# Performance work log

Measured on AMD Instinct MI355X. Metric: run time of the kernel, lower is better.

The kernel has to match this reference:

```python
import jax, jax.numpy as jnp
import numpy as np

B, N, F, FH, H = 8, 2048, 64, 64, 4
NEG_BIG = -1e10


def setup_inputs() -> dict:
    key = jax.random.key(0)
    k_x, k_a, k_w, k_as, k_an = jax.random.split(key, 5)
    X = jax.random.normal(k_x, (B, N, F), dtype=jnp.float32)
    A = (jax.random.uniform(k_a, (B, N, N)) < 0.1).astype(jnp.float32)
    A = jnp.maximum(A, jnp.eye(N, dtype=jnp.float32)[None])
    W = jax.random.normal(k_w, (H, F, FH), dtype=jnp.float32) * (1.0 / np.sqrt(F))
    b = jnp.zeros((H, FH), dtype=jnp.float32)
    a_self = jax.random.normal(k_as, (H, FH), dtype=jnp.float32) * (1.0 / np.sqrt(FH))
    a_neigh = jax.random.normal(k_an, (H, FH), dtype=jnp.float32) * (1.0 / np.sqrt(FH))
    return {"X": X, "A": A, "W": W, "b": b, "a_self": a_self, "a_neigh": a_neigh}


def reference(X, A, W, b, a_self, a_neigh):
    # per-head linear projection: [B,H,N,FH]
    feats = jnp.einsum("bnf,hfo->bhno", X, W)
    # additive attention logits: e_ij = leaky_relu(a_s.h_i + a_n.h_j)
    s_self = jnp.einsum("bhno,ho->bhn", feats, a_self)   # [B,H,N]
    s_neigh = jnp.einsum("bhno,ho->bhn", feats, a_neigh)  # [B,H,N]
    scores = s_self[:, :, :, None] + s_neigh[:, :, None, :]  # [B,H,N,N]
    scores = jax.nn.leaky_relu(scores, negative_slope=0.2)
    scores = scores + (1.0 - A)[:, None] * NEG_BIG  # adjacency mask
    attn = jax.nn.softmax(scores, axis=-1)
    # weighted aggregation + bias (dropouts are identity at inference)
    out = jnp.einsum("bhnm,bhmo->bhno", attn, feats) + b[None, :, None, :]
    # concat heads -> [B,N,H*FH], then activation
    Bd, Hd, Nd, Fd = out.shape
    out = jnp.transpose(out, (0, 2, 1, 3)).reshape(Bd, Nd, Hd * Fd)
    return jax.nn.relu(out)
```

## Files before the change

### kernel.cpp

```cpp
#include <hip/hip_runtime.h>
#include <hip/hip_bf16.h>
#include <stdint.h>

#define B_ 8
#define N_ 2048
#define F_ 64
#define FH_ 64
#define H_ 4
#define C_ (H_*FH_)
#define CHUNK 64
#define NCHUNK (N_/CHUNK)
#define LOG2E 1.44269504088896340736f

typedef short short8 __attribute__((ext_vector_type(8)));
typedef float f32x4 __attribute__((ext_vector_type(4)));

__device__ __forceinline__ short f2bf(float f) {
    __hip_bfloat16 h = __float2bfloat16(f);
    return __builtin_bit_cast(short, h);
}

__device__ __forceinline__ void async16(void* l, const void* g) {
    __builtin_amdgcn_global_load_lds((const __attribute__((address_space(1))) unsigned int*)g,
                                     (__attribute__((address_space(3))) unsigned int*)l, 16, 0, 0);
}
__device__ __forceinline__ void async4(void* l, const void* g) {
    __builtin_amdgcn_global_load_lds((const __attribute__((address_space(1))) unsigned int*)g,
                                     (__attribute__((address_space(3))) unsigned int*)l, 4, 0, 0);
}

__global__ __launch_bounds__(256) void k0_wt(const float* __restrict__ W,
                                             __hip_bfloat16* __restrict__ WT) {
    int idx = blockIdx.x * 256 + threadIdx.x;
    int h = idx >> 12, rem = idx & 4095, o = rem >> 6, f = rem & 63;
    WT[idx] = __float2bfloat16(W[(h * F_ + f) * FH_ + o]);
}

__global__ __launch_bounds__(256) void kp_pack(const float* __restrict__ A,
                                               unsigned long long* __restrict__ Amask) {
    const int wave = threadIdx.x >> 6, lane = threadIdx.x & 63;
    const int R = blockIdx.x * 4 + wave;
    const float* arow = A + (size_t)R * N_;
    unsigned long long* mrow = Amask + (size_t)R * (N_ / 64);
#pragma unroll
    for (int i = 0; i < 8; ++i) {
        float a0 = arow[i * 256 + lane];
        float a1 = arow[i * 256 + 64 + lane];
        float a2 = arow[i * 256 + 128 + lane];
        float a3 = arow[i * 256 + 192 + lane];
        unsigned long long m0 = __ballot(a0 != 0.0f);
        unsigned long long m1 = __ballot(a1 != 0.0f);
        unsigned long long m2 = __ballot(a2 != 0.0f);
        unsigned long long m3 = __ballot(a3 != 0.0f);
        if (lane == 0) {
            mrow[i * 4 + 0] = m0; mrow[i * 4 + 1] = m1;
            mrow[i * 4 + 2] = m2; mrow[i * 4 + 3] = m3;
        }
    }
}

__global__ __launch_bounds__(256) void k1_feats(const float* __restrict__ X,
                                                const __hip_bfloat16* __restrict__ WT,
                                                const float* __restrict__ a_self,
                                                const float* __restrict__ a_neigh,
                                                __hip_bfloat16* __restrict__ featsT,
                                                float* __restrict__ ss,
                                                float* __restrict__ sn) {
    __shared__ float a_lds[2][FH_];
    __shared__ __hip_bfloat16 c_lds[FH_ * 72];
    const int nb = blockIdx.x, h = blockIdx.y, b = blockIdx.z;
    const int tid = threadIdx.x;
    if (tid < 64)       a_lds[0][tid] = a_self[h * FH_ + tid];
    else if (tid < 128) a_lds[1][tid - 64] = a_neigh[h * FH_ + tid - 64];
    __syncthreads();

    const int wave = tid >> 6, lane = tid & 63;
    const int m = lane & 15, q = lane >> 4;
    const int nl = wave * 16 + m;
    const int n = nb * 64 + nl;
    f32x4 acc[4] = {};
#pragma unroll
    for (int ks = 0; ks < 2; ++ks) {
        const float* xp = X + ((size_t)(b * N_ + n)) * F_ + ks * 32 + q * 8;
        float4 x0 = *(const float4*)xp;
        float4 x1 = *(const float4*)(xp + 4);
        short8 bfrag;
        bfrag[0] = f2bf(x0.x); bfrag[1] = f2bf(x0.y);
        bfrag[2] = f2bf(x0.z); bfrag[3] = f2bf(x0.w);
        bfrag[4] = f2bf(x1.x); bfrag[5] = f2bf(x1.y);
        bfrag[6] = f2bf(x1.z); bfrag[7] = f2bf(x1.w);
#pragma unroll
        for (int ot = 0; ot < 4; ++ot) {
            short8 afrag = *(const short8*)(WT + ((size_t)(h * FH_ + ot * 16 + m)) * F_ + ks * 32 + q * 8);
            acc[ot] = __builtin_amdgcn_mfma_f32_16x16x32_bf16(afrag, bfrag, acc[ot], 0, 0, 0);
        }
    }
    float ssv = 0.f, snv = 0.f;
#pragma unroll
    for (int ot = 0; ot < 4; ++ot) {
#pragma unroll
        for (int r = 0; r < 4; ++r) {
            int orow = ot * 16 + q * 4 + r;
            float v = acc[ot][r];
            c_lds[orow * 72 + nl] = __float2bfloat16(v);
            ssv += v * a_lds[0][orow];
            snv += v * a_lds[1][orow];
        }
    }
    ssv += __shfl_xor(ssv, 16); ssv += __shfl_xor(ssv, 32);
    snv += __shfl_xor(snv, 16); snv += __shfl_xor(snv, 32);
    __syncthreads();
    {
        int o = tid >> 2, c = (tid & 3) * 16;
        const __hip_bfloat16* src = c_lds + o * 72 + c;
        __hip_bfloat16* dst = featsT + ((size_t)(b * H_ + h) * FH_ + o) * N_ + nb * 64 + c;
        *(uint4*)dst       = *(const uint4*)src;
        *(uint4*)(dst + 8) = *(const uint4*)(src + 8);
    }
    if (lane < 16) {
        size_t idx = ((size_t)(b * H_ + h)) * N_ + n;
        ss[idx] = ssv * LOG2E;
        sn[idx] = snv * LOG2E;
    }
}

__global__ __launch_bounds__(256, 4) void k3_attn(const unsigned int* __restrict__ Amask,
                                                  const __hip_bfloat16* __restrict__ featsT,
                                                  const float* __restrict__ ss,
                                                  const float* __restrict__ sn,
                                                  const float* __restrict__ bias,
                                                  float* __restrict__ out) {
    __shared__ __hip_bfloat16 fv_lds[2][64 * CHUNK];
    __shared__ unsigned int   mk_lds[2][64 * 2];
    __shared__ float e1_lds[N_];
    __shared__ float e2_lds[N_];

    const int tile = blockIdx.x, h = blockIdx.y, b = blockIdx.z;
    const int tid = threadIdx.x, wave = tid >> 6, lane = tid & 63;
    const int m = lane & 15, q = lane >> 4;
    const int rowtile = tile * 64;

    {
        const float4* snrow = (const float4*)(sn + ((size_t)(b * H_ + h)) * N_);
        float4* e1v = (float4*)e1_lds;
        float4* e2v = (float4*)e2_lds;
#pragma unroll
        for (int i = 0; i < 2; ++i) {
            int idx = tid + i * 256;
            float4 v = snrow[idx];
            float4 u1, u2;
            u1.x = exp2f(v.x); u1.y = exp2f(v.y); u1.z = exp2f(v.z); u1.w = exp2f(v.w);
            u2.x = exp2f(0.2f * v.x); u2.y = exp2f(0.2f * v.y);
            u2.z = exp2f(0.2f * v.z); u2.w = exp2f(0.2f * v.w);
            e1v[idx] = u1; e2v[idx] = u2;
        }
    }
    const float ssi = ss[((size_t)(b * H_ + h)) * N_ + rowtile + wave * 16 + m];
    const float e1i = exp2f(ssi), e2i = exp2f(0.2f * ssi);

    const __hip_bfloat16* fhead = featsT + ((size_t)(b * H_ + h)) * FH_ * N_;
    const unsigned int* mbase = Amask + ((size_t)(b * N_) + rowtile) * (N_ / 32);

    auto stage = [&](int c, int bufi) {
        const int cb = c * CHUNK;
#pragma unroll
        for (int i = 0; i < 2; ++i) {
            int base_unit = i * 256 + wave * 64;
            int unit = base_unit + lane;
            int o = unit >> 3, v = unit & 7;
            int u = v ^ (o & 7);
            async16(&fv_lds[bufi][base_unit * 8], fhead + (size_t)o * N_ + cb + u * 8);
        }
        if (wave < 2) {
            int base_unit = wave * 64;
            int unit = base_unit + lane;
            int row = unit >> 1, dw = unit & 1;
            async4(&mk_lds[bufi][base_unit], mbase + (size_t)row * (N_ / 32) + (cb >> 5) + dw);
        }
    };

    stage(0, 0);
    __syncthreads();

    f32x4 acc[2][4] = {};
    f32x4 accl[2] = {};
    short8 ones;
#pragma unroll
    for (int s = 0; s < 8; ++s) ones[s] = (short)0x3F80;

    for (int c = 0; c < NCHUNK; ++c) {
        const int cur = c & 1;
        if (c + 1 < NCHUNK) stage(c + 1, cur ^ 1);

        const int cg = c * CHUNK;
        float4 eA10 = *(const float4*)(e1_lds + cg + q * 8);
        float4 eA11 = *(const float4*)(e1_lds + cg + q * 8 + 4);
        float4 eB10 = *(const float4*)(e1_lds + cg + 32 + q * 8);
        float4 eB11 = *(const float4*)(e1_lds + cg + 32 + q * 8 + 4);
        float4 eA20 = *(const float4*)(e2_lds + cg + q * 8);
        float4 eA21 = *(const float4*)(e2_lds + cg + q * 8 + 4);
        float4 eB20 = *(const float4*)(e2_lds + cg + 32 + q * 8);
        float4 eB21 = *(const float4*)(e2_lds + cg + 32 + q * 8 + 4);
        short8 fA[4], fB[4];
#pragma unroll
        for (int ct = 0; ct < 4; ++ct) {
            int o = ct * 16 + m;
            fA[ct] = *(const short8*)(fv_lds[cur] + ((o << 3) + (q ^ (o & 7))) * 8);
            fB[ct] = *(const short8*)(fv_lds[cur] + ((o << 3) + ((4 + q) ^ (o & 7))) * 8);
        }
        unsigned int mA = mk_lds[cur][(wave * 16 + m) * 2];
        unsigned int mB = mk_lds[cur][(wave * 16 + m) * 2 + 1];

        float e1A[8] = {eA10.x, eA10.y, eA10.z, eA10.w, eA11.x, eA11.y, eA11.z, eA11.w};
        float e1B[8] = {eB10.x, eB10.y, eB10.z, eB10.w, eB11.x, eB11.y, eB11.z, eB11.w};
        float e2A[8] = {eA20.x, eA20.y, eA20.z, eA20.w, eA21.x, eA21.y, eA21.z, eA21.w};
        float e2B[8] = {eB20.x, eB20.y, eB20.z, eB20.w, eB21.x, eB21.y, eB21.z, eB21.w};

        short8 pA, pB;
#pragma unroll
        for (int s = 0; s < 8; ++s) {
            float vA = fmaxf(e1i * e1A[s], e2i * e2A[s]);
            float vB = fmaxf(e1i * e1B[s], e2i * e2B[s]);
            const int bit = q * 8 + s;
            pA[s] = (mA >> bit) & 1 ? f2bf(vA) : (short)0;
            pB[s] = (mB >> bit) & 1 ? f2bf(vB) : (short)0;
        }
#pragma unroll
        for (int ct = 0; ct < 4; ++ct) {
            acc[0][ct] = __builtin_amdgcn_mfma_f32_16x16x32_bf16(pA, fA[ct], acc[0][ct], 0, 0, 0);
            acc[1][ct] = __builtin_amdgcn_mfma_f32_16x16x32_bf16(pB, fB[ct], acc[1][ct], 0, 0, 0);
        }
        accl[0] = __builtin_amdgcn_mfma_f32_16x16x32_bf16(pA, ones, accl[0], 0, 0, 0);
        accl[1] = __builtin_amdgcn_mfma_f32_16x16x32_bf16(pB, ones, accl[1], 0, 0, 0);

        __syncthreads();
    }

    float bc[4];
#pragma unroll
    for (int ct = 0; ct < 4; ++ct) bc[ct] = bias[h * FH_ + ct * 16 + m];

#pragma unroll
    for (int r = 0; r < 4; ++r) {
        float inv = 1.0f / (accl[0][r] + accl[1][r]);
        int gr = rowtile + wave * 16 + q * 4 + r;
#pragma unroll
        for (int ct = 0; ct < 4; ++ct) {
            float v = (acc[0][ct][r] + acc[1][ct][r]) * inv + bc[ct];
            out[((size_t)(b * N_) + gr) * C_ + h * FH_ + ct * 16 + m] = fmaxf(v, 0.0f);
        }
    }
}

extern "C" void kernel_launch(void* const* d_in, const int* in_sizes, int n_in,
                              void* d_out, int out_size, void* d_ws, size_t ws_size,
                              hipStream_t stream) {
    const float* X       = (const float*)d_in[0];
    const float* A       = (const float*)d_in[1];
    const float* W       = (const float*)d_in[2];
    const float* bias    = (const float*)d_in[3];
    const float* a_self  = (const float*)d_in[4];
    const float* a_neigh = (const float*)d_in[5];
    float* out = (float*)d_out;

    char* ws = (char*)d_ws;
    __hip_bfloat16* featsT = (__hip_bfloat16*)(ws);
    __hip_bfloat16* WT     = (__hip_bfloat16*)(ws + 8388608);
    float* ss              = (float*)(ws + 8421376);
    float* sn              = (float*)(ws + 8683520);
    unsigned long long* Am = (unsigned long long*)(ws + 8945664);

    k0_wt    <<<64, 256, 0, stream>>>(W, WT);
    kp_pack  <<<B_ * N_ / 4, 256, 0, stream>>>(A, Am);
    k1_feats <<<dim3(N_ / 64, H_, B_), 256, 0, stream>>>(X, WT, a_self, a_neigh, featsT, ss, sn);
    k3_attn  <<<dim3(N_ / 64, H_, B_), 256, 0, stream>>>((const unsigned int*)Am, featsT, ss, sn, bias, out);
}
```

Measured before the change: 258.4 us.

## Give each wave private double-buffered LDS tiles and drop block barriers

Splits the four waves of the attention kernel into a 2x2 grid of row halves and feature halves. Each wave now stages its own 32-feature slice and its own mask rows into a private double buffer in LDS, and waits on its loads with an explicit vmcnt wait instead of a per-chunk __syncthreads. This removes block-wide synchronisation from the main loop and lets waves run out of step with each other. The cost is duplicated global and LDS traffic, probability computation repeated across the two feature-half waves, more LDS per block, and a lower occupancy hint (launch bounds 4 to 3).

```diff
diff --git a/kernel.cpp b/kernel.cpp
--- a/kernel.cpp
+++ b/kernel.cpp
@@ -14,6 +14,8 @@
 
 typedef short short8 __attribute__((ext_vector_type(8)));
 typedef float f32x4 __attribute__((ext_vector_type(4)));
+
+#define WAITVM(N) __builtin_amdgcn_s_waitcnt(((N)&15) | (7<<4) | (15<<8) | ((((N)>>4)&3)<<14))
 
 __device__ __forceinline__ short f2bf(float f) {
     __hip_bfloat16 h = __float2bfloat16(f);
@@ -124,20 +126,22 @@
     }
 }
 
-__global__ __launch_bounds__(256, 4) void k3_attn(const unsigned int* __restrict__ Amask,
+__global__ __launch_bounds__(256, 3) void k3_attn(const unsigned int* __restrict__ Amask,
                                                   const __hip_bfloat16* __restrict__ featsT,
                                                   const float* __restrict__ ss,
                                                   const float* __restrict__ sn,
                                                   const float* __restrict__ bias,
                                                   float* __restrict__ out) {
-    __shared__ __hip_bfloat16 fv_lds[2][64 * CHUNK];
-    __shared__ unsigned int   mk_lds[2][64 * 2];
+    __shared__ __hip_bfloat16 fv_lds[4][2][32 * CHUNK];
+    __shared__ unsigned int   mk_lds[4][2][64];
     __shared__ float e1_lds[N_];
     __shared__ float e2_lds[N_];
 
     const int tile = blockIdx.x, h = blockIdx.y, b = blockIdx.z;
     const int tid = threadIdx.x, wave = tid >> 6, lane = tid & 63;
     const int m = lane & 15, q = lane >> 4;
+    const int rh = wave >> 1;
+    const int fh = wave & 1;
     const int rowtile = tile * 64;
 
     {
@@ -155,43 +159,42 @@
             e1v[idx] = u1; e2v[idx] = u2;
         }
     }
-    const float ssi = ss[((size_t)(b * H_ + h)) * N_ + rowtile + wave * 16 + m];
-    const float e1i = exp2f(ssi), e2i = exp2f(0.2f * ssi);
-
-    const __hip_bfloat16* fhead = featsT + ((size_t)(b * H_ + h)) * FH_ * N_;
-    const unsigned int* mbase = Amask + ((size_t)(b * N_) + rowtile) * (N_ / 32);
+    const size_t srow = ((size_t)(b * H_ + h)) * N_ + rowtile + rh * 32 + m;
+    const float ssi0 = ss[srow], ssi1 = ss[srow + 16];
+    const float e1i[2] = {exp2f(ssi0), exp2f(ssi1)};
+    const float e2i[2] = {exp2f(0.2f * ssi0), exp2f(0.2f * ssi1)};
+
+    const __hip_bfloat16* fhead = featsT + (((size_t)(b * H_ + h)) * FH_ + fh * 32) * N_;
+    const unsigned int* mbase = Amask + ((size_t)(b * N_) + rowtile + rh * 32) * (N_ / 32);
+
+    __hip_bfloat16* fvw[2] = {&fv_lds[wave][0][0], &fv_lds[wave][1][0]};
+    unsigned int*   mkw[2] = {&mk_lds[wave][0][0], &mk_lds[wave][1][0]};
 
     auto stage = [&](int c, int bufi) {
         const int cb = c * CHUNK;
 #pragma unroll
-        for (int i = 0; i < 2; ++i) {
-            int base_unit = i * 256 + wave * 64;
-            int unit = base_unit + lane;
+        for (int i = 0; i < 4; ++i) {
+            int unit = i * 64 + lane;
             int o = unit >> 3, v = unit & 7;
             int u = v ^ (o & 7);
-            async16(&fv_lds[bufi][base_unit * 8], fhead + (size_t)o * N_ + cb + u * 8);
-        }
-        if (wave < 2) {
-            int base_unit = wave * 64;
-            int unit = base_unit + lane;
-            int row = unit >> 1, dw = unit & 1;
-            async4(&mk_lds[bufi][base_unit], mbase + (size_t)row * (N_ / 32) + (cb >> 5) + dw);
+            async16(fvw[bufi] + (size_t)(i * 64) * 8, fhead + (size_t)o * N_ + cb + u * 8);
+        }
+        {
+            int row = lane >> 1, dw = lane & 1;
+            async4(mkw[bufi], mbase + (size_t)row * (N_ / 32) + (cb >> 5) + dw);
         }
     };
 
     stage(0, 0);
     __syncthreads();
 
-    f32x4 acc[2][4] = {};
+    f32x4 acc[2][2] = {};
     f32x4 accl[2] = {};
     short8 ones;
 #pragma unroll
     for (int s = 0; s < 8; ++s) ones[s] = (short)0x3F80;
 
-    for (int c = 0; c < NCHUNK; ++c) {
-        const int cur = c & 1;
-        if (c + 1 < NCHUNK) stage(c + 1, cur ^ 1);
-
+    auto compute = [&](int c, int cur) {
         const int cg = c * CHUNK;
         float4 eA10 = *(const float4*)(e1_lds + cg + q * 8);
         float4 eA11 = *(const float4*)(e1_lds + cg + q * 8 + 4);
@@ -201,53 +204,66 @@
         float4 eA21 = *(const float4*)(e2_lds + cg + q * 8 + 4);
         float4 eB20 = *(const float4*)(e2_lds + cg + 32 + q * 8);
         float4 eB21 = *(const float4*)(e2_lds + cg + 32 + q * 8 + 4);
-        short8 fA[4], fB[4];
-#pragma unroll
-        for (int ct = 0; ct < 4; ++ct) {
-            int o = ct * 16 + m;
-            fA[ct] = *(const short8*)(fv_lds[cur] + ((o << 3) + (q ^ (o & 7))) * 8);
-            fB[ct] = *(const short8*)(fv_lds[cur] + ((o << 3) + ((4 + q) ^ (o & 7))) * 8);
-        }
-        unsigned int mA = mk_lds[cur][(wave * 16 + m) * 2];
-        unsigned int mB = mk_lds[cur][(wave * 16 + m) * 2 + 1];
-
+        short8 fA[2], fB[2];
+#pragma unroll
+        for (int ctl = 0; ctl < 2; ++ctl) {
+            int o = ctl * 16 + m;
+            fA[ctl] = *(const short8*)(fvw[cur] + ((o << 3) + (q ^ (o & 7))) * 8);
+            fB[ctl] = *(const short8*)(fvw[cur] + ((o << 3) + ((4 + q) ^ (o & 7))) * 8);
+        }
         float e1A[8] = {eA10.x, eA10.y, eA10.z, eA10.w, eA11.x, eA11.y, eA11.z, eA11.w};
         float e1B[8] = {eB10.x, eB10.y, eB10.z, eB10.w, eB11.x, eB11.y, eB11.z, eB11.w};
         float e2A[8] = {eA20.x, eA20.y, eA20.z, eA20.w, eA21.x, eA21.y, eA21.z, eA21.w};
         float e2B[8] = {eB20.x, eB20.y, eB20.z, eB20.w, eB21.x, eB21.y, eB21.z, eB21.w};
 
-        short8 pA, pB;
-#pragma unroll
-        for (int s = 0; s < 8; ++s) {
-            float vA = fmaxf(e1i * e1A[s], e2i * e2A[s]);
-            float vB = fmaxf(e1i * e1B[s], e2i * e2B[s]);
-            const int bit = q * 8 + s;
-            pA[s] = (mA >> bit) & 1 ? f2bf(vA) : (short)0;
-            pB[s] = (mB >> bit) & 1 ? f2bf(vB) : (short)0;
-        }
-#pragma unroll
-        for (int ct = 0; ct < 4; ++ct) {
-            acc[0][ct] = __builtin_amdgcn_mfma_f32_16x16x32_bf16(pA, fA[ct], acc[0][ct], 0, 0, 0);
-            acc[1][ct] = __builtin_amdgcn_mfma_f32_16x16x32_bf16(pB, fB[ct], acc[1][ct], 0, 0, 0);
-        }
-        accl[0] = __builtin_amdgcn_mfma_f32_16x16x32_bf16(pA, ones, accl[0], 0, 0, 0);
-        accl[1] = __builtin_amdgcn_mfma_f32_16x16x32_bf16(pB, ones, accl[1], 0, 0, 0);
-
-        __syncthreads();
-    }
-
-    float bc[4];
-#pragma unroll
-    for (int ct = 0; ct < 4; ++ct) bc[ct] = bias[h * FH_ + ct * 16 + m];
-
-#pragma unroll
-    for (int r = 0; r < 4; ++r) {
-        float inv = 1.0f / (accl[0][r] + accl[1][r]);
-        int gr = rowtile + wave * 16 + q * 4 + r;
-#pragma unroll
-        for (int ct = 0; ct < 4; ++ct) {
-            float v = (acc[0][ct][r] + acc[1][ct][r]) * inv + bc[ct];
-            out[((size_t)(b * N_) + gr) * C_ + h * FH_ + ct * 16 + m] = fmaxf(v, 0.0f);
+#pragma unroll
+        for (int st = 0; st < 2; ++st) {
+            unsigned int mA = mkw[cur][(st * 16 + m) * 2];
+            unsigned int mB = mkw[cur][(st * 16 + m) * 2 + 1];
+            short8 pA, pB;
+#pragma unroll
+            for (int s = 0; s < 8; ++s) {
+                float vA = fmaxf(e1i[st] * e1A[s], e2i[st] * e2A[s]);
+                float vB = fmaxf(e1i[st] * e1B[s], e2i[st] * e2B[s]);
+                const int bit = q * 8 + s;
+                pA[s] = (mA >> bit) & 1 ? f2bf(vA) : (short)0;
+                pB[s] = (mB >> bit) & 1 ? f2bf(vB) : (short)0;
+            }
+#pragma unroll
+            for (int ctl = 0; ctl < 2; ++ctl) {
+                acc[st][ctl] = __builtin_amdgcn_mfma_f32_16x16x32_bf16(pA, fA[ctl], acc[st][ctl], 0, 0, 0);
+                acc[st][ctl] = __builtin_amdgcn_mfma_f32_16x16x32_bf16(pB, fB[ctl], acc[st][ctl], 0, 0, 0);
+            }
+            accl[st] = __builtin_amdgcn_mfma_f32_16x16x32_bf16(pA, ones, accl[st], 0, 0, 0);
+            accl[st] = __builtin_amdgcn_mfma_f32_16x16x32_bf16(pB, ones, accl[st], 0, 0, 0);
+        }
+    };
+
+    for (int c = 0; c < NCHUNK - 1; ++c) {
+        stage(c + 1, (c + 1) & 1);
+        WAITVM(5);
+        __builtin_amdgcn_sched_barrier(0);
+        compute(c, c & 1);
+    }
+    WAITVM(0);
+    __builtin_amdgcn_sched_barrier(0);
+    compute(NCHUNK - 1, (NCHUNK - 1) & 1);
+
+    float bc[2];
+#pragma unroll
+    for (int ctl = 0; ctl < 2; ++ctl) bc[ctl] = bias[h * FH_ + fh * 32 + ctl * 16 + m];
+
+#pragma unroll
+    for (int st = 0; st < 2; ++st) {
+#pragma unroll
+        for (int r = 0; r < 4; ++r) {
+            float inv = 1.0f / accl[st][r];
+            int gr = rowtile + rh * 32 + st * 16 + q * 4 + r;
+#pragma unroll
+            for (int ctl = 0; ctl < 2; ++ctl) {
+                float v = acc[st][ctl][r] * inv + bc[ctl];
+                out[((size_t)(b * N_) + gr) * C_ + h * FH_ + fh * 32 + ctl * 16 + m] = fmaxf(v, 0.0f);
+            }
         }
     }
 }
```

Result: slower. 287.8 us (+11.4%).

## Triple-buffer attention chunk loads with explicit vmcnt waits and cheaper bf16 packing

Applied to the files above, without the earlier changes.

Moves the attention kernel from a double-buffered to a triple-buffered async global-to-LDS pipeline, prefetching two chunks ahead. Each iteration ends with a manual vmcnt wait and raw barrier instead of __syncthreads, so a later load can stay in flight across the barrier. The mask and bf16 conversion are rewritten as branch-free bit masking with a round-half-up add and byte-permute packing. Occupancy hint drops from 4 to 3 blocks per CU because of the extra LDS buffer. The rounding differs slightly from the original f2bf, and the hand-set waitcnt must match the number of outstanding loads per wave.

```diff
diff --git a/kernel.cpp b/kernel.cpp
--- a/kernel.cpp
+++ b/kernel.cpp
@@ -14,6 +14,9 @@
 
 typedef short short8 __attribute__((ext_vector_type(8)));
 typedef float f32x4 __attribute__((ext_vector_type(4)));
+typedef int   i32x4 __attribute__((ext_vector_type(4)));
+
+#define WAITVM(N) __builtin_amdgcn_s_waitcnt(((N)&15) | (7<<4) | (15<<8) | ((((N)>>4)&3)<<14))
 
 __device__ __forceinline__ short f2bf(float f) {
     __hip_bfloat16 h = __float2bfloat16(f);
@@ -124,21 +127,45 @@
     }
 }
 
-__global__ __launch_bounds__(256, 4) void k3_attn(const unsigned int* __restrict__ Amask,
+__global__ __launch_bounds__(256, 3) void k3_attn(const unsigned int* __restrict__ Amask,
                                                   const __hip_bfloat16* __restrict__ featsT,
                                                   const float* __restrict__ ss,
                                                   const float* __restrict__ sn,
                                                   const float* __restrict__ bias,
                                                   float* __restrict__ out) {
-    __shared__ __hip_bfloat16 fv_lds[2][64 * CHUNK];
-    __shared__ unsigned int   mk_lds[2][64 * 2];
-    __shared__ float e1_lds[N_];
-    __shared__ float e2_lds[N_];
+    __shared__ __attribute__((aligned(16))) __hip_bfloat16 fv_lds[3][64 * CHUNK];
+    __shared__ __attribute__((aligned(16))) unsigned int   mk_lds[3][128];
+    __shared__ __attribute__((aligned(16))) float e1_lds[N_];
+    __shared__ __attribute__((aligned(16))) float e2_lds[N_];
 
     const int tile = blockIdx.x, h = blockIdx.y, b = blockIdx.z;
     const int tid = threadIdx.x, wave = tid >> 6, lane = tid & 63;
     const int m = lane & 15, q = lane >> 4;
     const int rowtile = tile * 64;
+
+    const __hip_bfloat16* fhead = featsT + ((size_t)(b * H_ + h)) * FH_ * N_;
+    const unsigned int* mbase = Amask + ((size_t)(b * N_) + rowtile) * (N_ / 32);
+
+    auto stage = [&](int c, int bufi) {
+        const int cb = c * CHUNK;
+#pragma unroll
+        for (int i = 0; i < 2; ++i) {
+            int base_slot = wave * 128 + i * 64;
+            int slot = base_slot + lane;
+            int o = slot >> 3, vs = slot & 7;
+            int ug = vs ^ (o & 7);
+            async16(&fv_lds[bufi][base_slot * 8], fhead + (size_t)o * N_ + cb + ug * 8);
+        }
+        {
+            int base_slot = (wave & 1) * 64;
+            int slot = base_slot + lane;
+            int row = slot >> 1, dw = slot & 1;
+            async4(&mk_lds[bufi][base_slot], mbase + (size_t)row * (N_ / 32) + (cb >> 5) + dw);
+        }
+    };
+
+    stage(0, 0);
+    stage(1, 1);
 
     {
         const float4* snrow = (const float4*)(sn + ((size_t)(b * H_ + h)) * N_);
@@ -158,28 +185,6 @@
     const float ssi = ss[((size_t)(b * H_ + h)) * N_ + rowtile + wave * 16 + m];
     const float e1i = exp2f(ssi), e2i = exp2f(0.2f * ssi);
 
-    const __hip_bfloat16* fhead = featsT + ((size_t)(b * H_ + h)) * FH_ * N_;
-    const unsigned int* mbase = Amask + ((size_t)(b * N_) + rowtile) * (N_ / 32);
-
-    auto stage = [&](int c, int bufi) {
-        const int cb = c * CHUNK;
-#pragma unroll
-        for (int i = 0; i < 2; ++i) {
-            int base_unit = i * 256 + wave * 64;
-            int unit = base_unit + lane;
-            int o = unit >> 3, v = unit & 7;
-            int u = v ^ (o & 7);
-            async16(&fv_lds[bufi][base_unit * 8], fhead + (size_t)o * N_ + cb + u * 8);
-        }
-        if (wave < 2) {
-            int base_unit = wave * 64;
-            int unit = base_unit + lane;
-            int row = unit >> 1, dw = unit & 1;
-            async4(&mk_lds[bufi][base_unit], mbase + (size_t)row * (N_ / 32) + (cb >> 5) + dw);
-        }
-    };
-
-    stage(0, 0);
     __syncthreads();
 
     f32x4 acc[2][4] = {};
@@ -188,10 +193,7 @@
 #pragma unroll
     for (int s = 0; s < 8; ++s) ones[s] = (short)0x3F80;
 
-    for (int c = 0; c < NCHUNK; ++c) {
-        const int cur = c & 1;
-        if (c + 1 < NCHUNK) stage(c + 1, cur ^ 1);
-
+    auto compute = [&](int c, int cur) {
         const int cg = c * CHUNK;
         float4 eA10 = *(const float4*)(e1_lds + cg + q * 8);
         float4 eA11 = *(const float4*)(e1_lds + cg + q * 8 + 4);
@@ -208,23 +210,34 @@
             fA[ct] = *(const short8*)(fv_lds[cur] + ((o << 3) + (q ^ (o & 7))) * 8);
             fB[ct] = *(const short8*)(fv_lds[cur] + ((o << 3) + ((4 + q) ^ (o & 7))) * 8);
         }
-        unsigned int mA = mk_lds[cur][(wave * 16 + m) * 2];
-        unsigned int mB = mk_lds[cur][(wave * 16 + m) * 2 + 1];
+        uint2 md = *(const uint2*)&mk_lds[cur][(wave * 16 + m) * 2];
+        unsigned int mAq = md.x >> (q * 8);
+        unsigned int mBq = md.y >> (q * 8);
 
         float e1A[8] = {eA10.x, eA10.y, eA10.z, eA10.w, eA11.x, eA11.y, eA11.z, eA11.w};
         float e1B[8] = {eB10.x, eB10.y, eB10.z, eB10.w, eB11.x, eB11.y, eB11.z, eB11.w};
         float e2A[8] = {eA20.x, eA20.y, eA20.z, eA20.w, eA21.x, eA21.y, eA21.z, eA21.w};
         float e2B[8] = {eB20.x, eB20.y, eB20.z, eB20.w, eB21.x, eB21.y, eB21.z, eB21.w};
 
-        short8 pA, pB;
+        unsigned int uA[8], uB[8];
 #pragma unroll
         for (int s = 0; s < 8; ++s) {
             float vA = fmaxf(e1i * e1A[s], e2i * e2A[s]);
             float vB = fmaxf(e1i * e1B[s], e2i * e2B[s]);
-            const int bit = q * 8 + s;
-            pA[s] = (mA >> bit) & 1 ? f2bf(vA) : (short)0;
-            pB[s] = (mB >> bit) & 1 ? f2bf(vB) : (short)0;
-        }
+            int selA = ((int)(mAq << (31 - s))) >> 31;
+            int selB = ((int)(mBq << (31 - s))) >> 31;
+            uA[s] = (__float_as_uint(vA) + 0x8000u) & (unsigned int)selA;
+            uB[s] = (__float_as_uint(vB) + 0x8000u) & (unsigned int)selB;
+        }
+        i32x4 wa, wb;
+#pragma unroll
+        for (int d = 0; d < 4; ++d) {
+            wa[d] = (int)__builtin_amdgcn_perm(uA[2 * d + 1], uA[2 * d], 0x07060302u);
+            wb[d] = (int)__builtin_amdgcn_perm(uB[2 * d + 1], uB[2 * d], 0x07060302u);
+        }
+        short8 pA = __builtin_bit_cast(short8, wa);
+        short8 pB = __builtin_bit_cast(short8, wb);
+
 #pragma unroll
         for (int ct = 0; ct < 4; ++ct) {
             acc[0][ct] = __builtin_amdgcn_mfma_f32_16x16x32_bf16(pA, fA[ct], acc[0][ct], 0, 0, 0);
@@ -232,8 +245,15 @@
         }
         accl[0] = __builtin_amdgcn_mfma_f32_16x16x32_bf16(pA, ones, accl[0], 0, 0, 0);
         accl[1] = __builtin_amdgcn_mfma_f32_16x16x32_bf16(pB, ones, accl[1], 0, 0, 0);
-
-        __syncthreads();
+    };
+
+    for (int c = 0; c < NCHUNK; ++c) {
+        const bool more = (c + 2 < NCHUNK);
+        if (more) stage(c + 2, (c + 2) % 3);
+        compute(c, c % 3);
+        if (more) { WAITVM(3); } else { WAITVM(0); }
+        __builtin_amdgcn_s_barrier();
+        __builtin_amdgcn_sched_barrier(0);
     }
 
     float bc[4];
```

Measured after the change: 276.2 us. +6.9%, slower.

## Fuse weight transpose, mask packing and feature projection into one launch

Applied to the files above, without the earlier changes.

Merges the weight-transpose, adjacency-mask packing and feature-projection kernels into a single launch. Blocks past index 1024 pack the mask and the rest compute features. Each feature block now transposes its head's W slice into LDS itself instead of reading a precomputed WT buffer. This removes two kernel launches and the WT round trip, at the cost of redundant W conversion per block and an extra barrier for LDS reuse.

```diff
diff --git a/kernel.cpp b/kernel.cpp
--- a/kernel.cpp
+++ b/kernel.cpp
@@ -29,52 +29,56 @@
                                      (__attribute__((address_space(3))) unsigned int*)l, 4, 0, 0);
 }
 
-__global__ __launch_bounds__(256) void k0_wt(const float* __restrict__ W,
-                                             __hip_bfloat16* __restrict__ WT) {
-    int idx = blockIdx.x * 256 + threadIdx.x;
-    int h = idx >> 12, rem = idx & 4095, o = rem >> 6, f = rem & 63;
-    WT[idx] = __float2bfloat16(W[(h * F_ + f) * FH_ + o]);
-}
-
-__global__ __launch_bounds__(256) void kp_pack(const float* __restrict__ A,
-                                               unsigned long long* __restrict__ Amask) {
-    const int wave = threadIdx.x >> 6, lane = threadIdx.x & 63;
-    const int R = blockIdx.x * 4 + wave;
-    const float* arow = A + (size_t)R * N_;
-    unsigned long long* mrow = Amask + (size_t)R * (N_ / 64);
-#pragma unroll
-    for (int i = 0; i < 8; ++i) {
-        float a0 = arow[i * 256 + lane];
-        float a1 = arow[i * 256 + 64 + lane];
-        float a2 = arow[i * 256 + 128 + lane];
-        float a3 = arow[i * 256 + 192 + lane];
-        unsigned long long m0 = __ballot(a0 != 0.0f);
-        unsigned long long m1 = __ballot(a1 != 0.0f);
-        unsigned long long m2 = __ballot(a2 != 0.0f);
-        unsigned long long m3 = __ballot(a3 != 0.0f);
-        if (lane == 0) {
-            mrow[i * 4 + 0] = m0; mrow[i * 4 + 1] = m1;
-            mrow[i * 4 + 2] = m2; mrow[i * 4 + 3] = m3;
-        }
-    }
-}
-
-__global__ __launch_bounds__(256) void k1_feats(const float* __restrict__ X,
-                                                const __hip_bfloat16* __restrict__ WT,
-                                                const float* __restrict__ a_self,
-                                                const float* __restrict__ a_neigh,
-                                                __hip_bfloat16* __restrict__ featsT,
-                                                float* __restrict__ ss,
-                                                float* __restrict__ sn) {
+__global__ __launch_bounds__(256) void kf(const float* __restrict__ A,
+                                          const float* __restrict__ X,
+                                          const float* __restrict__ W,
+                                          const float* __restrict__ a_self,
+                                          const float* __restrict__ a_neigh,
+                                          unsigned long long* __restrict__ Amask,
+                                          __hip_bfloat16* __restrict__ featsT,
+                                          float* __restrict__ ss,
+                                          float* __restrict__ sn) {
     __shared__ float a_lds[2][FH_];
-    __shared__ __hip_bfloat16 c_lds[FH_ * 72];
-    const int nb = blockIdx.x, h = blockIdx.y, b = blockIdx.z;
+    __shared__ __hip_bfloat16 cw_lds[FH_ * 72];
+    const int bx = blockIdx.x;
     const int tid = threadIdx.x;
+    const int wave = tid >> 6, lane = tid & 63;
+
+    if (bx >= 1024) {
+        const int R = (bx - 1024) * 4 + wave;
+        const float* arow = A + (size_t)R * N_;
+        unsigned long long* mrow = Amask + (size_t)R * (N_ / 64);
+#pragma unroll
+        for (int i = 0; i < 8; ++i) {
+            float a0 = arow[i * 256 + lane];
+            float a1 = arow[i * 256 + 64 + lane];
+            float a2 = arow[i * 256 + 128 + lane];
+            float a3 = arow[i * 256 + 192 + lane];
+            unsigned long long m0 = __ballot(a0 != 0.0f);
+            unsigned long long m1 = __ballot(a1 != 0.0f);
+            unsigned long long m2 = __ballot(a2 != 0.0f);
+            unsigned long long m3 = __ballot(a3 != 0.0f);
+            if (lane == 0) {
+                mrow[i * 4 + 0] = m0; mrow[i * 4 + 1] = m1;
+                mrow[i * 4 + 2] = m2; mrow[i * 4 + 3] = m3;
+            }
+        }
+        return;
+    }
+
+    const int nb = bx & 31, h = (bx >> 5) & 3, b = bx >> 7;
+
     if (tid < 64)       a_lds[0][tid] = a_self[h * FH_ + tid];
     else if (tid < 128) a_lds[1][tid - 64] = a_neigh[h * FH_ + tid - 64];
-    __syncthreads();
-
-    const int wave = tid >> 6, lane = tid & 63;
+    {
+        int f = tid >> 2, o0 = (tid & 3) * 16;
+        const float* wsrc = W + ((size_t)(h * F_ + f)) * FH_ + o0;
+#pragma unroll
+        for (int k = 0; k < 16; ++k)
+            cw_lds[(o0 + k) * 72 + f] = __float2bfloat16(wsrc[k]);
+    }
+    __syncthreads();
+
     const int m = lane & 15, q = lane >> 4;
     const int nl = wave * 16 + m;
     const int n = nb * 64 + nl;
@@ -91,10 +95,11 @@
         bfrag[6] = f2bf(x1.z); bfrag[7] = f2bf(x1.w);
 #pragma unroll
         for (int ot = 0; ot < 4; ++ot) {
-            short8 afrag = *(const short8*)(WT + ((size_t)(h * FH_ + ot * 16 + m)) * F_ + ks * 32 + q * 8);
+            short8 afrag = *(const short8*)(cw_lds + (ot * 16 + m) * 72 + ks * 32 + q * 8);
             acc[ot] = __builtin_amdgcn_mfma_f32_16x16x32_bf16(afrag, bfrag, acc[ot], 0, 0, 0);
         }
     }
+    __syncthreads();
     float ssv = 0.f, snv = 0.f;
 #pragma unroll
     for (int ot = 0; ot < 4; ++ot) {
@@ -102,7 +107,7 @@
         for (int r = 0; r < 4; ++r) {
             int orow = ot * 16 + q * 4 + r;
             float v = acc[ot][r];
-            c_lds[orow * 72 + nl] = __float2bfloat16(v);
+            cw_lds[orow * 72 + nl] = __float2bfloat16(v);
             ssv += v * a_lds[0][orow];
             snv += v * a_lds[1][orow];
         }
@@ -112,7 +117,7 @@
     __syncthreads();
     {
         int o = tid >> 2, c = (tid & 3) * 16;
-        const __hip_bfloat16* src = c_lds + o * 72 + c;
+        const __hip_bfloat16* src = cw_lds + o * 72 + c;
         __hip_bfloat16* dst = featsT + ((size_t)(b * H_ + h) * FH_ + o) * N_ + nb * 64 + c;
         *(uint4*)dst       = *(const uint4*)src;
         *(uint4*)(dst + 8) = *(const uint4*)(src + 8);
@@ -265,13 +270,10 @@
 
     char* ws = (char*)d_ws;
     __hip_bfloat16* featsT = (__hip_bfloat16*)(ws);
-    __hip_bfloat16* WT     = (__hip_bfloat16*)(ws + 8388608);
     float* ss              = (float*)(ws + 8421376);
     float* sn              = (float*)(ws + 8683520);
     unsigned long long* Am = (unsigned long long*)(ws + 8945664);
 
-    k0_wt    <<<64, 256, 0, stream>>>(W, WT);
-    kp_pack  <<<B_ * N_ / 4, 256, 0, stream>>>(A, Am);
-    k1_feats <<<dim3(N_ / 64, H_, B_), 256, 0, stream>>>(X, WT, a_self, a_neigh, featsT, ss, sn);
-    k3_attn  <<<dim3(N_ / 64, H_, B_), 256, 0, stream>>>((const unsigned int*)Am, featsT, ss, sn, bias, out);
-}
+    kf      <<<5120, 256, 0, stream>>>(A, X, W, a_self, a_neigh, Am, featsT, ss, sn);
+    k3_attn <<<dim3(N_ / 64, H_, B_), 256, 0, stream>>>((const unsigned int*)Am, featsT, ss, sn, bias, out);
+}
```

Result: faster. 252.3 us (-2.4%).
